# Optimization experiments

Measured on AMD Instinct MI355X. Metric: run time of the kernel, lower is better.

Reference implementation:

```python
import jax, jax.numpy as jnp
import numpy as np

OUT_F = 11008
IN_F = 4096
BATCH = 4


def setup_inputs() -> dict:
    key = jax.random.key(0)
    k1, k2, k3, k4 = jax.random.split(key, 4)
    x = jax.random.normal(k1, (BATCH, IN_F), dtype=jnp.float32)
    # quantized int8 weight values live in [-127, 127]; stored as int32 here
    q_weight = jax.random.randint(k2, (OUT_F, IN_F), -127, 128, dtype=jnp.int32)
    # per-output-channel scales (positive, like abs_max / qmax)
    scales = jax.random.uniform(k3, (OUT_F,), dtype=jnp.float32, minval=0.001, maxval=0.05)
    bias = jax.random.normal(k4, (OUT_F,), dtype=jnp.float32)
    return {"x": x, "q_weight": q_weight, "scales": scales, "bias": bias}


def reference(x, q_weight, scales, bias):
    # dequantize: int8 weight * per-row scale -> fp32 weight [OUT_F, IN_F]
    dq_weight = q_weight.astype(jnp.float32) * scales[:, None]
    # F.linear: x @ W^T + b
    out = jnp.einsum("bi,oi->bo", x, dq_weight) + bias
    return out
```

## Files before the change

### kernel.cpp

```cpp
#include <hip/hip_runtime.h>

namespace {

constexpr int OUT_F = 11008;
constexpr int IN_F  = 4096;

typedef int   int4v   __attribute__((ext_vector_type(4)));
typedef float float4v __attribute__((ext_vector_type(4)));

constexpr int ROWS_PER_WAVE   = 2;
constexpr int WAVES_PER_BLOCK = 4;
constexpr int ROWS_PER_BLOCK  = ROWS_PER_WAVE * WAVES_PER_BLOCK;
constexpr int K_STEPS         = IN_F / (64 * 4);
constexpr int CHUNK           = 4;
constexpr int NCHUNK          = K_STEPS / CHUNK;

__global__ __launch_bounds__(256, 4) void qlinear_kernel(
    const float* __restrict__ x,
    const int*   __restrict__ qw,
    const float* __restrict__ scales,
    const float* __restrict__ bias,
    float*       __restrict__ out)
{
    __shared__ float4v xs[4 * (IN_F / 4)];

    const int tid = threadIdx.x;
    const float4v* xg = (const float4v*)x;
#pragma unroll
    for (int j = 0; j < (4 * IN_F / 4) / 256; ++j)
        xs[j * 256 + tid] = xg[j * 256 + tid];
    __syncthreads();

    const int lane = tid & 63;
    const int wid  = tid >> 6;
    const int row0 = blockIdx.x * ROWS_PER_BLOCK + wid * ROWS_PER_WAVE;

    const int4v* wp0 = (const int4v*)(qw + (size_t)row0 * IN_F);
    const int4v* wp1 = (const int4v*)(qw + (size_t)(row0 + 1) * IN_F);

    float acc[ROWS_PER_WAVE][4];
#pragma unroll
    for (int r = 0; r < ROWS_PER_WAVE; ++r)
#pragma unroll
        for (int b = 0; b < 4; ++b)
            acc[r][b] = 0.0f;

    int4v wa[ROWS_PER_WAVE][CHUNK], wb[ROWS_PER_WAVE][CHUNK];

#pragma unroll
    for (int s = 0; s < CHUNK; ++s) {
        wa[0][s] = wp0[s * 64 + lane];
        wa[1][s] = wp1[s * 64 + lane];
    }

#pragma unroll
    for (int c = 0; c < NCHUNK; ++c) {
        if (c + 1 < NCHUNK) {
#pragma unroll
            for (int s = 0; s < CHUNK; ++s) {
                wb[0][s] = wp0[((c + 1) * CHUNK + s) * 64 + lane];
                wb[1][s] = wp1[((c + 1) * CHUNK + s) * 64 + lane];
            }
        }

#pragma unroll
        for (int s = 0; s < CHUNK; ++s) {
            const int k = c * CHUNK + s;
            float4v xv[4];
#pragma unroll
            for (int b = 0; b < 4; ++b)
                xv[b] = xs[b * (IN_F / 4) + k * 64 + lane];

#pragma unroll
            for (int r = 0; r < ROWS_PER_WAVE; ++r) {
                float4v wf;
                wf.x = (float)wa[r][s].x;
                wf.y = (float)wa[r][s].y;
                wf.z = (float)wa[r][s].z;
                wf.w = (float)wa[r][s].w;
#pragma unroll
                for (int b = 0; b < 4; ++b) {
                    acc[r][b] += wf.x * xv[b].x;
                    acc[r][b] += wf.y * xv[b].y;
                    acc[r][b] += wf.z * xv[b].z;
                    acc[r][b] += wf.w * xv[b].w;
                }
            }
        }

        if (c + 1 < NCHUNK) {
#pragma unroll
            for (int s = 0; s < CHUNK; ++s) {
                wa[0][s] = wb[0][s];
                wa[1][s] = wb[1][s];
            }
        }
    }

#pragma unroll
    for (int r = 0; r < ROWS_PER_WAVE; ++r)
#pragma unroll
        for (int b = 0; b < 4; ++b) {
            float v = acc[r][b];
#pragma unroll
            for (int m = 32; m >= 1; m >>= 1)
                v += __shfl_xor(v, m, 64);
            acc[r][b] = v;
        }

    if (lane == 0) {
#pragma unroll
        for (int r = 0; r < ROWS_PER_WAVE; ++r) {
            const int row = row0 + r;
            const float s  = scales[row];
            const float bz = bias[row];
#pragma unroll
            for (int b = 0; b < 4; ++b)
                out[(size_t)b * OUT_F + row] = acc[r][b] * s + bz;
        }
    }
}

}

extern "C" void kernel_launch(void* const* d_in, const int* in_sizes, int n_in,
                              void* d_out, int out_size, void* d_ws, size_t ws_size,
                              hipStream_t stream) {
    const float* x      = (const float*)d_in[0];
    const int*   qw     = (const int*)d_in[1];
    const float* scales = (const float*)d_in[2];
    const float* bias   = (const float*)d_in[3];
    float*       out    = (float*)d_out;

    const int grid = OUT_F / ROWS_PER_BLOCK;
    qlinear_kernel<<<grid, 256, 0, stream>>>(x, qw, scales, bias, out);
}
```

Measured before the change: 34.14 us.

## Double-buffer x slices in shared memory, overlapped with weight prefetch

The kernel no longer copies the whole activation matrix into shared memory and synchronizes before issuing any weight loads. Instead, x is staged in 1024-element K-slices into a two-buffer shared array. The next slice is loaded alongside the next weight chunk, with one barrier per slice. This cuts the shared-memory footprint per block, which may allow more resident blocks, and hides the startup x load behind weight traffic. The cost is extra barriers inside the K loop and larger per-slice register prefetch buffers.

```diff
diff --git a/kernel.cpp b/kernel.cpp
--- a/kernel.cpp
+++ b/kernel.cpp
@@ -11,9 +11,10 @@
 constexpr int ROWS_PER_WAVE   = 2;
 constexpr int WAVES_PER_BLOCK = 4;
 constexpr int ROWS_PER_BLOCK  = ROWS_PER_WAVE * WAVES_PER_BLOCK;
-constexpr int K_STEPS         = IN_F / (64 * 4);
-constexpr int CHUNK           = 4;
-constexpr int NCHUNK          = K_STEPS / CHUNK;
+constexpr int SLICE_K         = 1024;
+constexpr int NSLICE          = IN_F / SLICE_K;
+constexpr int STEPS           = SLICE_K / 256;
+constexpr int SLICE_F4        = SLICE_K / 4;
 
 __global__ __launch_bounds__(256, 4) void qlinear_kernel(
     const float* __restrict__ x,
@@ -22,21 +23,16 @@
     const float* __restrict__ bias,
     float*       __restrict__ out)
 {
-    __shared__ float4v xs[4 * (IN_F / 4)];
+    __shared__ float4v xs[2][4 * SLICE_F4];
 
-    const int tid = threadIdx.x;
-    const float4v* xg = (const float4v*)x;
-#pragma unroll
-    for (int j = 0; j < (4 * IN_F / 4) / 256; ++j)
-        xs[j * 256 + tid] = xg[j * 256 + tid];
-    __syncthreads();
-
+    const int tid  = threadIdx.x;
     const int lane = tid & 63;
     const int wid  = tid >> 6;
     const int row0 = blockIdx.x * ROWS_PER_BLOCK + wid * ROWS_PER_WAVE;
 
-    const int4v* wp0 = (const int4v*)(qw + (size_t)row0 * IN_F);
-    const int4v* wp1 = (const int4v*)(qw + (size_t)(row0 + 1) * IN_F);
+    const float4v* xg  = (const float4v*)x;
+    const int4v*   wp0 = (const int4v*)(qw + (size_t)row0 * IN_F);
+    const int4v*   wp1 = (const int4v*)(qw + (size_t)(row0 + 1) * IN_F);
 
     float acc[ROWS_PER_WAVE][4];
 #pragma unroll
@@ -45,31 +41,46 @@
         for (int b = 0; b < 4; ++b)
             acc[r][b] = 0.0f;
 
-    int4v wa[ROWS_PER_WAVE][CHUNK], wb[ROWS_PER_WAVE][CHUNK];
+    int4v wa[ROWS_PER_WAVE][STEPS], wb[ROWS_PER_WAVE][STEPS];
+    {
+        float4v t[4];
+#pragma unroll
+        for (int j = 0; j < 4; ++j)
+            t[j] = xg[j * (IN_F / 4) + tid];
+#pragma unroll
+        for (int s = 0; s < STEPS; ++s) {
+            wa[0][s] = wp0[s * 64 + lane];
+            wa[1][s] = wp1[s * 64 + lane];
+        }
+#pragma unroll
+        for (int j = 0; j < 4; ++j)
+            xs[0][j * SLICE_F4 + tid] = t[j];
+    }
+    __syncthreads();
 
 #pragma unroll
-    for (int s = 0; s < CHUNK; ++s) {
-        wa[0][s] = wp0[s * 64 + lane];
-        wa[1][s] = wp1[s * 64 + lane];
-    }
-
+    for (int c = 0; c < NSLICE; ++c) {
+        if (c + 1 < NSLICE) {
+            float4v t[4];
 #pragma unroll
-    for (int c = 0; c < NCHUNK; ++c) {
-        if (c + 1 < NCHUNK) {
+            for (int j = 0; j < 4; ++j)
+                t[j] = xg[j * (IN_F / 4) + (c + 1) * SLICE_F4 + tid];
 #pragma unroll
-            for (int s = 0; s < CHUNK; ++s) {
-                wb[0][s] = wp0[((c + 1) * CHUNK + s) * 64 + lane];
-                wb[1][s] = wp1[((c + 1) * CHUNK + s) * 64 + lane];
+            for (int s = 0; s < STEPS; ++s) {
+                wb[0][s] = wp0[((c + 1) * STEPS + s) * 64 + lane];
+                wb[1][s] = wp1[((c + 1) * STEPS + s) * 64 + lane];
             }
+#pragma unroll
+            for (int j = 0; j < 4; ++j)
+                xs[(c + 1) & 1][j * SLICE_F4 + tid] = t[j];
         }
 
 #pragma unroll
-        for (int s = 0; s < CHUNK; ++s) {
-            const int k = c * CHUNK + s;
+        for (int s = 0; s < STEPS; ++s) {
             float4v xv[4];
 #pragma unroll
             for (int b = 0; b < 4; ++b)
-                xv[b] = xs[b * (IN_F / 4) + k * 64 + lane];
+                xv[b] = xs[c & 1][b * SLICE_F4 + s * 64 + lane];
 
 #pragma unroll
             for (int r = 0; r < ROWS_PER_WAVE; ++r) {
@@ -88,9 +99,10 @@
             }
         }
 
-        if (c + 1 < NCHUNK) {
+        if (c + 1 < NSLICE) {
+            __syncthreads();
 #pragma unroll
-            for (int s = 0; s < CHUNK; ++s) {
+            for (int s = 0; s < STEPS; ++s) {
                 wa[0][s] = wb[0][s];
                 wa[1][s] = wb[1][s];
             }
```

Measured after the change: 33.86 us. About the same (-0.8%).
